# Kernel optimization log

Hardware: AMD Instinct MI355X
Metric: run time of the kernel (lower is better)

Reference implementation:

```python
import jax, jax.numpy as jnp
import numpy as np

DIM = 192
H = W = 128
HEADS = 6
HEAD_DIM = DIM // HEADS
WIN = 8
SHIFT = 4
B = 16
LN_EPS = 1e-5


def setup_inputs() -> dict:
    key = jax.random.key(0)
    ks = jax.random.split(key, 16)
    d = DIM
    s = lambda *sh: 1.0 / np.sqrt(sh[-1])
    inp = {
        "x": jax.random.normal(ks[0], (B, H * W, d), jnp.float32),
        # torch Linear layout: (out, in)
        "qkv_w": jax.random.normal(ks[1], (3 * d, d), jnp.float32) * s(d, d),
        "qkv_b": jnp.zeros((3 * d,), jnp.float32),
        "proj_w": jax.random.normal(ks[2], (d, d), jnp.float32) * s(d, d),
        "proj_b": jnp.zeros((d,), jnp.float32),
        "n1_g": jnp.ones((d,), jnp.float32),
        "n1_b": jnp.zeros((d,), jnp.float32),
        "n2_g": jnp.ones((d,), jnp.float32),
        "n2_b": jnp.zeros((d,), jnp.float32),
        "w1": jax.random.normal(ks[3], (4 * d, d), jnp.float32) * s(d, d),
        "b1": jnp.zeros((4 * d,), jnp.float32),
        "w2": jax.random.normal(ks[4], (d, 4 * d), jnp.float32) * s(d, 4 * d),
        "b2": jnp.zeros((d,), jnp.float32),
    }
    return inp


def _ln(x, g, b):
    m = jnp.mean(x, -1, keepdims=True)
    v = jnp.mean(jnp.square(x - m), -1, keepdims=True)
    return (x - m) * jax.lax.rsqrt(v + LN_EPS) * g + b


def _l2norm(x):
    n = jnp.sqrt(jnp.sum(jnp.square(x), -1, keepdims=True))
    return x / jnp.maximum(n, 1e-12)


def _swin_forward(x, qkv_w, qkv_b, proj_w, proj_b, n1_g, n1_b, n2_g, n2_b, w1, b1, w2, b2):
    Bq, L, C = x.shape
    shortcut = x
    h = _ln(x, n1_g, n1_b).reshape(Bq, H, W, C)
    h = jnp.roll(h, (-SHIFT, -SHIFT), axis=(1, 2))
    nH, nW = H // WIN, W // WIN
    hw = h.reshape(Bq, nH, WIN, nW, WIN, C).transpose(0, 1, 3, 2, 4, 5)
    hw = hw.reshape(Bq * nH * nW, WIN * WIN, C)
    N = WIN * WIN
    qkv = hw @ qkv_w.T + qkv_b                      # (nWin, N, 3C)
    qkv = qkv.reshape(-1, N, 3, HEADS, HEAD_DIM).transpose(2, 0, 3, 1, 4)
    q, k, v = qkv[0], qkv[1], qkv[2]                # (nWin, heads, N, hd)
    q = _l2norm(q)
    k = _l2norm(k)
    scale = HEAD_DIM ** -0.5
    attn = jnp.einsum('whnd,whmd->whnm', q, k) * scale
    attn = attn - jnp.max(attn, -1, keepdims=True)
    attn = jax.nn.softmax(attn, -1)
    attn = jnp.clip(attn, 1e-6, 1.0)
    o = jnp.einsum('whnm,whmd->whnd', attn, v)      # (nWin, heads, N, hd)
    o = o.transpose(0, 2, 1, 3).reshape(-1, N, C)
    o = o @ proj_w.T + proj_b
    # window reverse
    o = o.reshape(Bq, nH, nW, WIN, WIN, C).transpose(0, 1, 3, 2, 4, 5)
    o = o.reshape(Bq, H, W, C)
    o = jnp.roll(o, (SHIFT, SHIFT), axis=(1, 2)).reshape(Bq, L, C)
    x = shortcut + o
    m = _ln(x, n2_g, n2_b)
    m = jax.nn.gelu(m @ w1.T + b1, approximate=False) @ w2.T + b2
    return x + m


def reference(x, qkv_w, qkv_b, proj_w, proj_b, n1_g, n1_b, n2_g, n2_b, w1, b1, w2, b2):
    return _swin_forward(x, qkv_w, qkv_b, proj_w, proj_b, n1_g, n1_b, n2_g, n2_b, w1, b1, w2, b2)
```

## Files before the change

kernel.cpp:

```cpp
#include <hip/hip_runtime.h>


typedef short s8v __attribute__((ext_vector_type(8)));
typedef float f4v __attribute__((ext_vector_type(4)));
typedef unsigned short u16;

static __device__ __forceinline__ float b2f(u16 u) {
    unsigned int x = ((unsigned int)u) << 16;
    return __builtin_bit_cast(float, x);
}
static __device__ __forceinline__ u16 f2b(float f) {
    unsigned int u = __builtin_bit_cast(unsigned int, f);
    u = (u + 0x7FFF + ((u >> 16) & 1)) >> 16;
    return (u16)u;
}
static __device__ __forceinline__ f4v mfma16(s8v a, s8v b, f4v c) {
    return __builtin_amdgcn_mfma_f32_16x16x32_bf16(a, b, c, 0, 0, 0);
}

#define SWZ(r, e) ((e) ^ (((r) & 7) << 3))

#define SZ_QKV  110592
#define SZ_PROJ  36864
#define SZ_W1   147456
#define SZ_W2   147456
#define OFF_PROJ (SZ_QKV)
#define OFF_W1   (SZ_QKV + SZ_PROJ)
#define OFF_W2   (SZ_QKV + SZ_PROJ + SZ_W1)
#define W_TOTAL  (SZ_QKV + SZ_PROJ + SZ_W1 + SZ_W2)

__global__ __launch_bounds__(256) void cvt_weights(
    const float* __restrict__ qkv_w, const float* __restrict__ proj_w,
    const float* __restrict__ w1, const float* __restrict__ w2,
    u16* __restrict__ dst)
{
    int i4 = (blockIdx.x * 256 + threadIdx.x) * 4;
    const float* src; int off;
    if (i4 < OFF_PROJ)     { src = qkv_w; off = i4; }
    else if (i4 < OFF_W1)  { src = proj_w; off = i4 - OFF_PROJ; }
    else if (i4 < OFF_W2)  { src = w1; off = i4 - OFF_W1; }
    else                   { src = w2; off = i4 - OFF_W2; }
    float4 v = *(const float4*)(src + off);
    ushort4 o;
    o.x = f2b(v.x); o.y = f2b(v.y); o.z = f2b(v.z); o.w = f2b(v.w);
    *(ushort4*)(dst + i4) = o;
}

__global__ __launch_bounds__(256, 3) void attn_fused(
    const float* __restrict__ x, const u16* __restrict__ Wqkv,
    const float* __restrict__ bqkv, const u16* __restrict__ Wproj,
    const float* __restrict__ bproj, const float* __restrict__ g1,
    const float* __restrict__ bn1, const float* __restrict__ g2,
    const float* __restrict__ bn2, u16* __restrict__ x2,
    u16* __restrict__ xln)
{
    __shared__ __align__(16) u16 lds[27136];
    u16* hs   = lds;
    u16* ks   = lds;
    u16* vt   = lds + 12288;
    u16* pscr = lds + 24576;

    const int tid = threadIdx.x;
    const int wv = tid >> 6, lane = tid & 63;
    const int lr = lane & 15, lq = lane >> 4;
    const int wloc = blockIdx.x;
    const int bb = wloc >> 8, wh = (wloc >> 4) & 15, ww = wloc & 15;
    u16* pw = pscr + wv * 640;

    {
        int tk = tid >> 2, q4 = tid & 3;
        int gh = (wh * 8 + (tk >> 3) + 4) & 127;
        int gw = (ww * 8 + (tk & 7) + 4) & 127;
        const float* xr = x + (((size_t)bb * 128 + gh) * 128 + gw) * 192 + q4 * 48;
        float4 xv[12];
        float s = 0.f, sq = 0.f;
#pragma unroll
        for (int i = 0; i < 12; i++) {
            xv[i] = *(const float4*)(xr + i * 4);
            s += xv[i].x + xv[i].y + xv[i].z + xv[i].w;
            sq += xv[i].x * xv[i].x + xv[i].y * xv[i].y
                + xv[i].z * xv[i].z + xv[i].w * xv[i].w;
        }
        s += __shfl_xor(s, 1); sq += __shfl_xor(sq, 1);
        s += __shfl_xor(s, 2); sq += __shfl_xor(sq, 2);
        float mean = s * (1.0f / 192.0f);
        float var = sq * (1.0f / 192.0f) - mean * mean;
        float rstd = 1.0f / sqrtf(var + 1e-5f);
#pragma unroll
        for (int i = 0; i < 12; i += 2) {
            int c0 = q4 * 48 + i * 4;
            float4 ga  = *(const float4*)(g1 + c0);
            float4 gb  = *(const float4*)(g1 + c0 + 4);
            float4 ba  = *(const float4*)(bn1 + c0);
            float4 bbv = *(const float4*)(bn1 + c0 + 4);
            s8v ov;
            ov[0] = (short)f2b((xv[i].x - mean) * rstd * ga.x + ba.x);
            ov[1] = (short)f2b((xv[i].y - mean) * rstd * ga.y + ba.y);
            ov[2] = (short)f2b((xv[i].z - mean) * rstd * ga.z + ba.z);
            ov[3] = (short)f2b((xv[i].w - mean) * rstd * ga.w + ba.w);
            ov[4] = (short)f2b((xv[i + 1].x - mean) * rstd * gb.x + bbv.x);
            ov[5] = (short)f2b((xv[i + 1].y - mean) * rstd * gb.y + bbv.y);
            ov[6] = (short)f2b((xv[i + 1].z - mean) * rstd * gb.z + bbv.z);
            ov[7] = (short)f2b((xv[i + 1].w - mean) * rstd * gb.w + bbv.w);
            *(s8v*)&hs[SWZ(tk, tk * 192 + c0)] = ov;
        }
    }
    __syncthreads();

    const int trow = 16 * wv + lr;
    s8v af[6];
#pragma unroll
    for (int k = 0; k < 6; k++)
        af[k] = *(const s8v*)&hs[SWZ(trow, trow * 192 + 32 * k + lq * 8)];
    __syncthreads();

    s8v aq[6];
#pragma unroll
    for (int h = 0; h < 6; h++) {
        f4v acc[6] = {};
#pragma unroll
        for (int k = 0; k < 6; k++) {
#pragma unroll
            for (int n = 0; n < 6; n++) {
                int wr = (n < 2) ? (32 * h + 16 * n + lr)
                       : (n < 4) ? (192 + 32 * h + 16 * (n - 2) + lr)
                                 : (384 + 32 * h + 16 * (n - 4) + lr);
                s8v bf = *(const s8v*)&Wqkv[(size_t)wr * 192 + 32 * k + lq * 8];
                acc[n] = mfma16(af[k], bf, acc[n]);
            }
        }
        float bq0 = bqkv[32 * h + lr],       bq1 = bqkv[32 * h + 16 + lr];
        float bk0 = bqkv[192 + 32 * h + lr], bk1 = bqkv[192 + 32 * h + 16 + lr];
        float bv0 = bqkv[384 + 32 * h + lr], bv1 = bqkv[384 + 32 * h + 16 + lr];
#pragma unroll
        for (int reg = 0; reg < 4; reg++) {
            int row = 16 * wv + lq * 4 + reg;
            float q0 = acc[0][reg] + bq0, q1 = acc[1][reg] + bq1;
            float ss = q0 * q0 + q1 * q1;
#pragma unroll
            for (int m = 1; m < 16; m <<= 1) ss += __shfl_xor(ss, m);
            float inv = 1.0f / fmaxf(sqrtf(ss), 1e-12f);
            pw[(lq * 4 + reg) * 40 + lr]      = f2b(q0 * inv);
            pw[(lq * 4 + reg) * 40 + 16 + lr] = f2b(q1 * inv);

            float k0v = acc[2][reg] + bk0, k1v = acc[3][reg] + bk1;
            ss = k0v * k0v + k1v * k1v;
#pragma unroll
            for (int m = 1; m < 16; m <<= 1) ss += __shfl_xor(ss, m);
            inv = 1.0f / fmaxf(sqrtf(ss), 1e-12f);
            ks[SWZ(row, row * 192 + 32 * h + lr)]      = f2b(k0v * inv);
            ks[SWZ(row, row * 192 + 32 * h + 16 + lr)] = f2b(k1v * inv);

            int d0 = 32 * h + lr, d1 = 32 * h + 16 + lr;
            vt[SWZ(d0, d0 * 64 + row)] = f2b(acc[4][reg] + bv0);
            vt[SWZ(d1, d1 * 64 + row)] = f2b(acc[5][reg] + bv1);
        }
        aq[h] = *(const s8v*)&pw[lr * 40 + lq * 8];
    }
    __syncthreads();

    f4v acc2[12] = {};
    const float scale = 0.17677669529663687f;
#pragma unroll
    for (int h = 0; h < 6; h++) {
        f4v accS[4] = {};
#pragma unroll
        for (int j = 0; j < 4; j++) {
            int kr = 16 * j + lr;
            s8v bk = *(const s8v*)&ks[SWZ(kr, kr * 192 + 32 * h + lq * 8)];
            accS[j] = mfma16(aq[h], bk, accS[j]);
        }
        float p[4][4];
#pragma unroll
        for (int reg = 0; reg < 4; reg++) {
            float v0 = accS[0][reg] * scale, v1 = accS[1][reg] * scale;
            float v2 = accS[2][reg] * scale, v3 = accS[3][reg] * scale;
            float mx = fmaxf(fmaxf(v0, v1), fmaxf(v2, v3));
#pragma unroll
            for (int m = 1; m < 16; m <<= 1) mx = fmaxf(mx, __shfl_xor(mx, m));
            float e0 = __expf(v0 - mx), e1 = __expf(v1 - mx);
            float e2 = __expf(v2 - mx), e3 = __expf(v3 - mx);
            float sum = e0 + e1 + e2 + e3;
#pragma unroll
            for (int m = 1; m < 16; m <<= 1) sum += __shfl_xor(sum, m);
            float is = 1.0f / sum;
            p[0][reg] = fminf(fmaxf(e0 * is, 1e-6f), 1.0f);
            p[1][reg] = fminf(fmaxf(e1 * is, 1e-6f), 1.0f);
            p[2][reg] = fminf(fmaxf(e2 * is, 1e-6f), 1.0f);
            p[3][reg] = fminf(fmaxf(e3 * is, 1e-6f), 1.0f);
        }
        f4v accO[2] = {};
#pragma unroll
        for (int reg = 0; reg < 4; reg++) {
            pw[(lq * 4 + reg) * 40 + lr]      = f2b(p[0][reg]);
            pw[(lq * 4 + reg) * 40 + 16 + lr] = f2b(p[1][reg]);
        }
        {
            s8v ap0 = *(const s8v*)&pw[lr * 40 + lq * 8];
#pragma unroll
            for (int n = 0; n < 2; n++) {
                int d = 32 * h + 16 * n + lr;
                s8v bvf = *(const s8v*)&vt[SWZ(d, d * 64 + lq * 8)];
                accO[n] = mfma16(ap0, bvf, accO[n]);
            }
        }
#pragma unroll
        for (int reg = 0; reg < 4; reg++) {
            pw[(lq * 4 + reg) * 40 + lr]      = f2b(p[2][reg]);
            pw[(lq * 4 + reg) * 40 + 16 + lr] = f2b(p[3][reg]);
        }
        {
            s8v ap1 = *(const s8v*)&pw[lr * 40 + lq * 8];
#pragma unroll
            for (int n = 0; n < 2; n++) {
                int d = 32 * h + 16 * n + lr;
                s8v bvf = *(const s8v*)&vt[SWZ(d, d * 64 + 32 + lq * 8)];
                accO[n] = mfma16(ap1, bvf, accO[n]);
            }
        }
#pragma unroll
        for (int n = 0; n < 2; n++)
#pragma unroll
            for (int reg = 0; reg < 4; reg++)
                pw[(lq * 4 + reg) * 40 + 16 * n + lr] = f2b(accO[n][reg]);
        s8v apj = *(const s8v*)&pw[lr * 40 + lq * 8];
#pragma unroll
        for (int n = 0; n < 12; n++) {
            s8v bpj = *(const s8v*)&Wproj[(size_t)(16 * n + lr) * 192 + 32 * h + lq * 8];
            acc2[n] = mfma16(apj, bpj, acc2[n]);
        }
    }

    float bpv[12], g2v[12], b2v[12];
#pragma unroll
    for (int n = 0; n < 12; n++) {
        int col = 16 * n + lr;
        bpv[n] = bproj[col]; g2v[n] = g2[col]; b2v[n] = bn2[col];
    }
#pragma unroll
    for (int reg = 0; reg < 4; reg++) {
        int tk = 16 * wv + lq * 4 + reg;
        int gh = (wh * 8 + (tk >> 3) + 4) & 127;
        int gw = (ww * 8 + (tk & 7) + 4) & 127;
        size_t base = (((size_t)bb * 128 + gh) * 128 + gw) * 192;
        float vv[12];
        float s = 0.f, sq = 0.f;
#pragma unroll
        for (int n = 0; n < 12; n++) {
            float v = acc2[n][reg] + bpv[n] + x[base + 16 * n + lr];
            vv[n] = v; s += v; sq += v * v;
        }
        s += __shfl_xor(s, 1); sq += __shfl_xor(sq, 1);
        s += __shfl_xor(s, 2); sq += __shfl_xor(sq, 2);
        s += __shfl_xor(s, 4); sq += __shfl_xor(sq, 4);
        s += __shfl_xor(s, 8); sq += __shfl_xor(sq, 8);
        float mean = s * (1.0f / 192.0f);
        float var = sq * (1.0f / 192.0f) - mean * mean;
        float rstd = 1.0f / sqrtf(var + 1e-5f);
#pragma unroll
        for (int n = 0; n < 12; n++) {
            size_t idx = base + 16 * n + lr;
            x2[idx]  = f2b(vv[n]);
            xln[idx] = f2b((vv[n] - mean) * rstd * g2v[n] + b2v[n]);
        }
    }
}

__global__ __launch_bounds__(256, 3) void mlp1_gemm(
    const u16* __restrict__ xln, const u16* __restrict__ W1,
    const float* __restrict__ B1, u16* __restrict__ mh, int ldm, int nchunk)
{
    __shared__ __align__(16) u16 As[128 * 200];
    const int tid = threadIdx.x;
    const int wv = tid >> 6, lane = tid & 63;
    const int lr = lane & 15, lq = lane >> 4;
    const size_t m0 = (size_t)blockIdx.x * 128;

    {
        int r = tid >> 1, hf = tid & 1;
        const u16* xr = xln + (m0 + r) * 192 + hf * 96;
        u16* ar = As + r * 200 + hf * 96;
#pragma unroll
        for (int i = 0; i < 12; i++)
            *(s8v*)(ar + i * 8) = *(const s8v*)(xr + i * 8);
    }
    __syncthreads();

    for (int c = 0; c < nchunk; c++) {
        f4v acc[2][12] = {};
        for (int k0 = 0; k0 < 192; k0 += 32) {
            s8v afr[2];
#pragma unroll
            for (int mt = 0; mt < 2; mt++)
                afr[mt] = *(const s8v*)&As[(32 * wv + 16 * mt + lr) * 200 + k0 + lq * 8];
#pragma unroll
            for (int n = 0; n < 12; n++) {
                s8v bf = *(const s8v*)&W1[(size_t)(c * 192 + 16 * n + lr) * 192 + k0 + lq * 8];
#pragma unroll
                for (int mt = 0; mt < 2; mt++)
                    acc[mt][n] = mfma16(afr[mt], bf, acc[mt][n]);
            }
        }
#pragma unroll
        for (int n = 0; n < 12; n++) {
            int col = c * 192 + 16 * n + lr;
            float bb = B1[col];
#pragma unroll
            for (int mt = 0; mt < 2; mt++)
#pragma unroll
                for (int reg = 0; reg < 4; reg++) {
                    size_t row = m0 + 32 * wv + 16 * mt + lq * 4 + reg;
                    float v = acc[mt][n][reg] + bb;
                    v = 0.5f * v * (1.0f + erff(v * 0.70710678118654752f));
                    mh[row * ldm + col] = f2b(v);
                }
        }
    }
}

#define BM 128
#define BN 64
#define LDT 40

template <int RES>
__global__ __launch_bounds__(256) void gemm_bt(
    const u16* __restrict__ A, int lda,
    const u16* __restrict__ W, int ldb,
    const float* __restrict__ bias,
    const u16* __restrict__ residB, const float* __restrict__ residF, int ldr,
    float* __restrict__ Cout, int ldc, int K)
{
    __shared__ __align__(16) u16 As[BM * LDT];
    __shared__ __align__(16) u16 Bs[BN * LDT];
    const int tid = threadIdx.x;
    const int wave = tid >> 6, lane = tid & 63;
    const int lr = lane & 15, lq = lane >> 4;
    const int wm = (wave >> 1) * 64;
    const int wn = (wave & 1) * 32;
    const size_t m0 = (size_t)blockIdx.y * BM;
    const int n0 = blockIdx.x * BN;

    const int ar = tid >> 1, ac = (tid & 1) * 16;
    const int br = tid >> 2, bc = (tid & 3) * 8;
    const u16* aptr = A + (m0 + ar) * (size_t)lda + ac;
    const u16* bptr = W + (size_t)(n0 + br) * ldb + bc;

    f4v acc[4][2] = {};
    for (int k0 = 0; k0 < K; k0 += 32) {
        __syncthreads();
        *(s8v*)&As[ar * LDT + ac]     = *(const s8v*)(aptr + k0);
        *(s8v*)&As[ar * LDT + ac + 8] = *(const s8v*)(aptr + k0 + 8);
        *(s8v*)&Bs[br * LDT + bc]     = *(const s8v*)(bptr + k0);
        __syncthreads();
        s8v af[4], bfr[2];
#pragma unroll
        for (int mt = 0; mt < 4; mt++)
            af[mt] = *(const s8v*)&As[(wm + mt * 16 + lr) * LDT + lq * 8];
#pragma unroll
        for (int nt = 0; nt < 2; nt++)
            bfr[nt] = *(const s8v*)&Bs[(wn + nt * 16 + lr) * LDT + lq * 8];
#pragma unroll
        for (int mt = 0; mt < 4; mt++)
#pragma unroll
            for (int nt = 0; nt < 2; nt++)
                acc[mt][nt] = mfma16(af[mt], bfr[nt], acc[mt][nt]);
    }

    float bv[2];
#pragma unroll
    for (int nt = 0; nt < 2; nt++) {
        int col = n0 + wn + nt * 16 + lr;
        bv[nt] = bias ? bias[col] : 0.0f;
    }
#pragma unroll
    for (int mt = 0; mt < 4; mt++)
#pragma unroll
        for (int reg = 0; reg < 4; reg++) {
            size_t row = m0 + wm + mt * 16 + lq * 4 + reg;
#pragma unroll
            for (int nt = 0; nt < 2; nt++) {
                int col = n0 + wn + nt * 16 + lr;
                float v = acc[mt][nt][reg] + bv[nt];
                if (RES == 1) v += b2f(residB[row * (size_t)ldr + col]);
                if (RES == 2) v += residF[row * (size_t)ldr + col];
                Cout[row * (size_t)ldc + col] = v;
            }
        }
}

extern "C" void kernel_launch(void* const* d_in, const int* in_sizes, int n_in,
                              void* d_out, int out_size, void* d_ws, size_t ws_size,
                              hipStream_t stream) {
    const float* x      = (const float*)d_in[0];
    const float* qkv_w  = (const float*)d_in[1];
    const float* qkv_b  = (const float*)d_in[2];
    const float* proj_w = (const float*)d_in[3];
    const float* proj_b = (const float*)d_in[4];
    const float* n1_g   = (const float*)d_in[5];
    const float* n1_b   = (const float*)d_in[6];
    const float* n2_g   = (const float*)d_in[7];
    const float* n2_b   = (const float*)d_in[8];
    const float* w1     = (const float*)d_in[9];
    const float* b1     = (const float*)d_in[10];
    const float* w2     = (const float*)d_in[11];
    const float* b2     = (const float*)d_in[12];
    float* out = (float*)d_out;

    u16* wsu = (u16*)d_ws;
    u16* wQ  = wsu;
    u16* wP  = wsu + OFF_PROJ;
    u16* wW1 = wsu + OFF_W1;
    u16* wW2 = wsu + OFF_W2;
    char* dataBase = (char*)d_ws + (1 << 20);
    size_t avail = (ws_size > (1 << 20)) ? ws_size - (1 << 20) : 0;

    dim3 blk(256);
    cvt_weights<<<W_TOTAL / 1024, blk, 0, stream>>>(qkv_w, proj_w, w1, w2, wsu);

    const size_t perTok = (size_t)(192 + 192 + 768) * 2;
    int Bs = 16;
    while (Bs > 1 && (size_t)Bs * 16384 * perTok > avail) Bs >>= 1;
    const bool bigHC = ((size_t)Bs * 16384 * perTok <= avail);

    if (bigHC) {
        const int nslice = 16 / Bs;
        const size_t stok = (size_t)Bs * 16384;
        u16* x2buf  = (u16*)dataBase;
        u16* xlnbuf = x2buf + stok * 192;
        u16* mhbuf  = xlnbuf + stok * 192;
        for (int s = 0; s < nslice; s++) {
            const float* xs = x + (size_t)s * stok * 192;
            float* outs = out + (size_t)s * stok * 192;
            attn_fused<<<Bs * 256, blk, 0, stream>>>(xs, wQ, qkv_b, wP, proj_b,
                                                     n1_g, n1_b, n2_g, n2_b,
                                                     x2buf, xlnbuf);
            mlp1_gemm<<<Bs * 128, blk, 0, stream>>>(xlnbuf, wW1, b1, mhbuf, 768, 4);
            gemm_bt<1><<<dim3(3, Bs * 128), blk, 0, stream>>>(
                mhbuf, 768, wW2, 768, b2, x2buf, nullptr, 192, outs, 192, 768);
        }
    } else {
        const size_t stok = 16384;
        u16* x2buf  = (u16*)dataBase;
        u16* xlnbuf = x2buf + stok * 192;
        u16* mhbuf  = xlnbuf + stok * 192;
        for (int s = 0; s < 16; s++) {
            const float* xs = x + (size_t)s * stok * 192;
            float* outs = out + (size_t)s * stok * 192;
            attn_fused<<<256, blk, 0, stream>>>(xs, wQ, qkv_b, wP, proj_b,
                                                n1_g, n1_b, n2_g, n2_b,
                                                x2buf, xlnbuf);
            for (int c = 0; c < 4; c++) {
                mlp1_gemm<<<128, blk, 0, stream>>>(
                    xlnbuf, wW1 + (size_t)c * 192 * 192, b1 + c * 192,
                    mhbuf, 192, 1);
                if (c == 0)
                    gemm_bt<1><<<dim3(3, 128), blk, 0, stream>>>(
                        mhbuf, 192, wW2 + c * 192, 768, b2,
                        x2buf, nullptr, 192, outs, 192, 192);
                else
                    gemm_bt<2><<<dim3(3, 128), blk, 0, stream>>>(
                        mhbuf, 192, wW2 + c * 192, 768, nullptr,
                        nullptr, outs, 192, outs, 192, 192);
            }
        }
    }
}
```

Baseline: 1.659 ms.

## Fuse MLP into one kernel and pipeline per-head attention with smaller LDS

The MLP's two GEMMs become a single kernel. It keeps the GELU hidden chunk in shared memory and accumulates the second GEMM in registers, so the large hidden activation buffer is no longer written to and read back from global memory. The attention kernel now processes heads in a software pipeline. It computes QKV for head h while running attention for head h-1, using double-buffered per-head K/V slices. This shrinks LDS so occupancy can go from 3 to 4 blocks per CU, at the cost of one block-wide barrier per head and weight reloads per 64-row MLP tile.

```diff
diff --git a/kernel.cpp b/kernel.cpp
--- a/kernel.cpp
+++ b/kernel.cpp
@@ -46,7 +46,125 @@
     *(ushort4*)(dst + i4) = o;
 }
 
-__global__ __launch_bounds__(256, 3) void attn_fused(
+static __device__ __forceinline__ void qkv_head(
+    int h, const s8v* af, const u16* __restrict__ Wqkv,
+    const float* __restrict__ bqkv, u16* kb, u16* vb, u16* qw,
+    s8v& aqOut, int wv, int lr, int lq)
+{
+    f4v acc[6] = {};
+#pragma unroll
+    for (int k = 0; k < 6; k++) {
+#pragma unroll
+        for (int n = 0; n < 6; n++) {
+            int wr = (n < 2) ? (32 * h + 16 * n + lr)
+                   : (n < 4) ? (192 + 32 * h + 16 * (n - 2) + lr)
+                             : (384 + 32 * h + 16 * (n - 4) + lr);
+            s8v bf = *(const s8v*)&Wqkv[(size_t)wr * 192 + 32 * k + lq * 8];
+            acc[n] = mfma16(af[k], bf, acc[n]);
+        }
+    }
+    float bq0 = bqkv[32 * h + lr],       bq1 = bqkv[32 * h + 16 + lr];
+    float bk0 = bqkv[192 + 32 * h + lr], bk1 = bqkv[192 + 32 * h + 16 + lr];
+    float bv0 = bqkv[384 + 32 * h + lr], bv1 = bqkv[384 + 32 * h + 16 + lr];
+#pragma unroll
+    for (int reg = 0; reg < 4; reg++) {
+        int row = 16 * wv + lq * 4 + reg;
+        float q0 = acc[0][reg] + bq0, q1 = acc[1][reg] + bq1;
+        float ss = q0 * q0 + q1 * q1;
+#pragma unroll
+        for (int m = 1; m < 16; m <<= 1) ss += __shfl_xor(ss, m);
+        float inv = 1.0f / fmaxf(sqrtf(ss), 1e-12f);
+        qw[(lq * 4 + reg) * 40 + lr]      = f2b(q0 * inv);
+        qw[(lq * 4 + reg) * 40 + 16 + lr] = f2b(q1 * inv);
+
+        float k0v = acc[2][reg] + bk0, k1v = acc[3][reg] + bk1;
+        ss = k0v * k0v + k1v * k1v;
+#pragma unroll
+        for (int m = 1; m < 16; m <<= 1) ss += __shfl_xor(ss, m);
+        inv = 1.0f / fmaxf(sqrtf(ss), 1e-12f);
+        kb[SWZ(row, row * 32 + lr)]      = f2b(k0v * inv);
+        kb[SWZ(row, row * 32 + 16 + lr)] = f2b(k1v * inv);
+
+        vb[SWZ(lr, lr * 64 + row)]             = f2b(acc[4][reg] + bv0);
+        vb[SWZ(16 + lr, (16 + lr) * 64 + row)] = f2b(acc[5][reg] + bv1);
+    }
+    aqOut = *(const s8v*)&qw[lr * 40 + lq * 8];
+}
+
+static __device__ __forceinline__ void attn_head(
+    int h, s8v aq, const u16* kb, const u16* vb, u16* pw,
+    f4v* acc2, const u16* __restrict__ Wproj, int wv, int lr, int lq)
+{
+    f4v accS[4] = {};
+#pragma unroll
+    for (int j = 0; j < 4; j++) {
+        int kr = 16 * j + lr;
+        s8v bk = *(const s8v*)&kb[SWZ(kr, kr * 32 + lq * 8)];
+        accS[j] = mfma16(aq, bk, accS[j]);
+    }
+    const float scale = 0.17677669529663687f;
+    float p[4][4];
+#pragma unroll
+    for (int reg = 0; reg < 4; reg++) {
+        float v0 = accS[0][reg] * scale, v1 = accS[1][reg] * scale;
+        float v2 = accS[2][reg] * scale, v3 = accS[3][reg] * scale;
+        float mx = fmaxf(fmaxf(v0, v1), fmaxf(v2, v3));
+#pragma unroll
+        for (int m = 1; m < 16; m <<= 1) mx = fmaxf(mx, __shfl_xor(mx, m));
+        float e0 = __expf(v0 - mx), e1 = __expf(v1 - mx);
+        float e2 = __expf(v2 - mx), e3 = __expf(v3 - mx);
+        float sum = e0 + e1 + e2 + e3;
+#pragma unroll
+        for (int m = 1; m < 16; m <<= 1) sum += __shfl_xor(sum, m);
+        float is = 1.0f / sum;
+        p[0][reg] = fminf(fmaxf(e0 * is, 1e-6f), 1.0f);
+        p[1][reg] = fminf(fmaxf(e1 * is, 1e-6f), 1.0f);
+        p[2][reg] = fminf(fmaxf(e2 * is, 1e-6f), 1.0f);
+        p[3][reg] = fminf(fmaxf(e3 * is, 1e-6f), 1.0f);
+    }
+    f4v accO[2] = {};
+#pragma unroll
+    for (int reg = 0; reg < 4; reg++) {
+        pw[(lq * 4 + reg) * 40 + lr]      = f2b(p[0][reg]);
+        pw[(lq * 4 + reg) * 40 + 16 + lr] = f2b(p[1][reg]);
+    }
+    {
+        s8v ap = *(const s8v*)&pw[lr * 40 + lq * 8];
+#pragma unroll
+        for (int n = 0; n < 2; n++) {
+            int d = 16 * n + lr;
+            s8v bvf = *(const s8v*)&vb[SWZ(d, d * 64 + lq * 8)];
+            accO[n] = mfma16(ap, bvf, accO[n]);
+        }
+    }
+#pragma unroll
+    for (int reg = 0; reg < 4; reg++) {
+        pw[(lq * 4 + reg) * 40 + lr]      = f2b(p[2][reg]);
+        pw[(lq * 4 + reg) * 40 + 16 + lr] = f2b(p[3][reg]);
+    }
+    {
+        s8v ap = *(const s8v*)&pw[lr * 40 + lq * 8];
+#pragma unroll
+        for (int n = 0; n < 2; n++) {
+            int d = 16 * n + lr;
+            s8v bvf = *(const s8v*)&vb[SWZ(d, d * 64 + 32 + lq * 8)];
+            accO[n] = mfma16(ap, bvf, accO[n]);
+        }
+    }
+#pragma unroll
+    for (int n = 0; n < 2; n++)
+#pragma unroll
+        for (int reg = 0; reg < 4; reg++)
+            pw[(lq * 4 + reg) * 40 + 16 * n + lr] = f2b(accO[n][reg]);
+    s8v apj = *(const s8v*)&pw[lr * 40 + lq * 8];
+#pragma unroll
+    for (int n = 0; n < 12; n++) {
+        s8v bpj = *(const s8v*)&Wproj[(size_t)(16 * n + lr) * 192 + 32 * h + lq * 8];
+        acc2[n] = mfma16(apj, bpj, acc2[n]);
+    }
+}
+
+__global__ __launch_bounds__(256, 4) void attn_fused(
     const float* __restrict__ x, const u16* __restrict__ Wqkv,
     const float* __restrict__ bqkv, const u16* __restrict__ Wproj,
     const float* __restrict__ bproj, const float* __restrict__ g1,
@@ -54,17 +172,17 @@
     const float* __restrict__ bn2, u16* __restrict__ x2,
     u16* __restrict__ xln)
 {
-    __shared__ __align__(16) u16 lds[27136];
+    __shared__ __align__(16) u16 lds[13312];
     u16* hs   = lds;
-    u16* ks   = lds;
-    u16* vt   = lds + 12288;
-    u16* pscr = lds + 24576;
+    u16* qscr = lds + 8192;
+    u16* pscr = lds + 10752;
 
     const int tid = threadIdx.x;
     const int wv = tid >> 6, lane = tid & 63;
     const int lr = lane & 15, lq = lane >> 4;
     const int wloc = blockIdx.x;
     const int bb = wloc >> 8, wh = (wloc >> 4) & 15, ww = wloc & 15;
+    u16* qw = qscr + wv * 640;
     u16* pw = pscr + wv * 640;
 
     {
@@ -105,8 +223,6 @@
             *(s8v*)&hs[SWZ(tk, tk * 192 + c0)] = ov;
         }
     }
-    __syncthreads();
-
     const int trow = 16 * wv + lr;
     s8v af[6];
 #pragma unroll
@@ -114,122 +230,21 @@
         af[k] = *(const s8v*)&hs[SWZ(trow, trow * 192 + 32 * k + lq * 8)];
     __syncthreads();
 
-    s8v aq[6];
+    f4v acc2[12] = {};
+    s8v aqv[6];
 #pragma unroll
     for (int h = 0; h < 6; h++) {
-        f4v acc[6] = {};
-#pragma unroll
-        for (int k = 0; k < 6; k++) {
-#pragma unroll
-            for (int n = 0; n < 6; n++) {
-                int wr = (n < 2) ? (32 * h + 16 * n + lr)
-                       : (n < 4) ? (192 + 32 * h + 16 * (n - 2) + lr)
-                                 : (384 + 32 * h + 16 * (n - 4) + lr);
-                s8v bf = *(const s8v*)&Wqkv[(size_t)wr * 192 + 32 * k + lq * 8];
-                acc[n] = mfma16(af[k], bf, acc[n]);
-            }
-        }
-        float bq0 = bqkv[32 * h + lr],       bq1 = bqkv[32 * h + 16 + lr];
-        float bk0 = bqkv[192 + 32 * h + lr], bk1 = bqkv[192 + 32 * h + 16 + lr];
-        float bv0 = bqkv[384 + 32 * h + lr], bv1 = bqkv[384 + 32 * h + 16 + lr];
-#pragma unroll
-        for (int reg = 0; reg < 4; reg++) {
-            int row = 16 * wv + lq * 4 + reg;
-            float q0 = acc[0][reg] + bq0, q1 = acc[1][reg] + bq1;
-            float ss = q0 * q0 + q1 * q1;
-#pragma unroll
-            for (int m = 1; m < 16; m <<= 1) ss += __shfl_xor(ss, m);
-            float inv = 1.0f / fmaxf(sqrtf(ss), 1e-12f);
-            pw[(lq * 4 + reg) * 40 + lr]      = f2b(q0 * inv);
-            pw[(lq * 4 + reg) * 40 + 16 + lr] = f2b(q1 * inv);
-
-            float k0v = acc[2][reg] + bk0, k1v = acc[3][reg] + bk1;
-            ss = k0v * k0v + k1v * k1v;
-#pragma unroll
-            for (int m = 1; m < 16; m <<= 1) ss += __shfl_xor(ss, m);
-            inv = 1.0f / fmaxf(sqrtf(ss), 1e-12f);
-            ks[SWZ(row, row * 192 + 32 * h + lr)]      = f2b(k0v * inv);
-            ks[SWZ(row, row * 192 + 32 * h + 16 + lr)] = f2b(k1v * inv);
-
-            int d0 = 32 * h + lr, d1 = 32 * h + 16 + lr;
-            vt[SWZ(d0, d0 * 64 + row)] = f2b(acc[4][reg] + bv0);
-            vt[SWZ(d1, d1 * 64 + row)] = f2b(acc[5][reg] + bv1);
-        }
-        aq[h] = *(const s8v*)&pw[lr * 40 + lq * 8];
-    }
-    __syncthreads();
-
-    f4v acc2[12] = {};
-    const float scale = 0.17677669529663687f;
-#pragma unroll
-    for (int h = 0; h < 6; h++) {
-        f4v accS[4] = {};
-#pragma unroll
-        for (int j = 0; j < 4; j++) {
-            int kr = 16 * j + lr;
-            s8v bk = *(const s8v*)&ks[SWZ(kr, kr * 192 + 32 * h + lq * 8)];
-            accS[j] = mfma16(aq[h], bk, accS[j]);
-        }
-        float p[4][4];
-#pragma unroll
-        for (int reg = 0; reg < 4; reg++) {
-            float v0 = accS[0][reg] * scale, v1 = accS[1][reg] * scale;
-            float v2 = accS[2][reg] * scale, v3 = accS[3][reg] * scale;
-            float mx = fmaxf(fmaxf(v0, v1), fmaxf(v2, v3));
-#pragma unroll
-            for (int m = 1; m < 16; m <<= 1) mx = fmaxf(mx, __shfl_xor(mx, m));
-            float e0 = __expf(v0 - mx), e1 = __expf(v1 - mx);
-            float e2 = __expf(v2 - mx), e3 = __expf(v3 - mx);
-            float sum = e0 + e1 + e2 + e3;
-#pragma unroll
-            for (int m = 1; m < 16; m <<= 1) sum += __shfl_xor(sum, m);
-            float is = 1.0f / sum;
-            p[0][reg] = fminf(fmaxf(e0 * is, 1e-6f), 1.0f);
-            p[1][reg] = fminf(fmaxf(e1 * is, 1e-6f), 1.0f);
-            p[2][reg] = fminf(fmaxf(e2 * is, 1e-6f), 1.0f);
-            p[3][reg] = fminf(fmaxf(e3 * is, 1e-6f), 1.0f);
-        }
-        f4v accO[2] = {};
-#pragma unroll
-        for (int reg = 0; reg < 4; reg++) {
-            pw[(lq * 4 + reg) * 40 + lr]      = f2b(p[0][reg]);
-            pw[(lq * 4 + reg) * 40 + 16 + lr] = f2b(p[1][reg]);
-        }
-        {
-            s8v ap0 = *(const s8v*)&pw[lr * 40 + lq * 8];
-#pragma unroll
-            for (int n = 0; n < 2; n++) {
-                int d = 32 * h + 16 * n + lr;
-                s8v bvf = *(const s8v*)&vt[SWZ(d, d * 64 + lq * 8)];
-                accO[n] = mfma16(ap0, bvf, accO[n]);
-            }
-        }
-#pragma unroll
-        for (int reg = 0; reg < 4; reg++) {
-            pw[(lq * 4 + reg) * 40 + lr]      = f2b(p[2][reg]);
-            pw[(lq * 4 + reg) * 40 + 16 + lr] = f2b(p[3][reg]);
-        }
-        {
-            s8v ap1 = *(const s8v*)&pw[lr * 40 + lq * 8];
-#pragma unroll
-            for (int n = 0; n < 2; n++) {
-                int d = 32 * h + 16 * n + lr;
-                s8v bvf = *(const s8v*)&vt[SWZ(d, d * 64 + 32 + lq * 8)];
-                accO[n] = mfma16(ap1, bvf, accO[n]);
-            }
-        }
-#pragma unroll
-        for (int n = 0; n < 2; n++)
-#pragma unroll
-            for (int reg = 0; reg < 4; reg++)
-                pw[(lq * 4 + reg) * 40 + 16 * n + lr] = f2b(accO[n][reg]);
-        s8v apj = *(const s8v*)&pw[lr * 40 + lq * 8];
-#pragma unroll
-        for (int n = 0; n < 12; n++) {
-            s8v bpj = *(const s8v*)&Wproj[(size_t)(16 * n + lr) * 192 + 32 * h + lq * 8];
-            acc2[n] = mfma16(apj, bpj, acc2[n]);
-        }
-    }
+        u16* kb = lds + ((h & 1) << 11);
+        u16* vb = lds + 4096 + ((h & 1) << 11);
+        qkv_head(h, af, Wqkv, bqkv, kb, vb, qw, aqv[h], wv, lr, lq);
+        if (h > 0) {
+            u16* kbp = lds + (((h - 1) & 1) << 11);
+            u16* vbp = lds + 4096 + (((h - 1) & 1) << 11);
+            attn_head(h - 1, aqv[h - 1], kbp, vbp, pw, acc2, Wproj, wv, lr, lq);
+        }
+        __syncthreads();
+    }
+    attn_head(5, aqv[5], lds + 2048, lds + 4096 + 2048, pw, acc2, Wproj, wv, lr, lq);
 
     float bpv[12], g2v[12], b2v[12];
 #pragma unroll
@@ -266,126 +281,77 @@
     }
 }
 
-__global__ __launch_bounds__(256, 3) void mlp1_gemm(
-    const u16* __restrict__ xln, const u16* __restrict__ W1,
-    const float* __restrict__ B1, u16* __restrict__ mh, int ldm, int nchunk)
+__global__ __launch_bounds__(256, 3) void mlp_fused(
+    const u16* __restrict__ xln, const u16* __restrict__ x2,
+    const u16* __restrict__ W1, const float* __restrict__ B1,
+    const u16* __restrict__ W2, const float* __restrict__ B2,
+    float* __restrict__ out)
 {
-    __shared__ __align__(16) u16 As[128 * 200];
+    __shared__ __align__(16) u16 lds[24576];
+    u16* As = lds;
+    u16* Ms = lds + 12288;
     const int tid = threadIdx.x;
     const int wv = tid >> 6, lane = tid & 63;
     const int lr = lane & 15, lq = lane >> 4;
-    const size_t m0 = (size_t)blockIdx.x * 128;
+    const size_t m0 = (size_t)blockIdx.x * 64;
 
     {
-        int r = tid >> 1, hf = tid & 1;
-        const u16* xr = xln + (m0 + r) * 192 + hf * 96;
-        u16* ar = As + r * 200 + hf * 96;
-#pragma unroll
-        for (int i = 0; i < 12; i++)
-            *(s8v*)(ar + i * 8) = *(const s8v*)(xr + i * 8);
+        int r = tid >> 2, q4 = tid & 3;
+        const u16* xr = xln + (m0 + r) * 192 + q4 * 48;
+        int ebase = r * 192 + q4 * 48;
+#pragma unroll
+        for (int i = 0; i < 6; i++)
+            *(s8v*)&As[SWZ(r, ebase + i * 8)] = *(const s8v*)(xr + i * 8);
     }
     __syncthreads();
 
-    for (int c = 0; c < nchunk; c++) {
-        f4v acc[2][12] = {};
-        for (int k0 = 0; k0 < 192; k0 += 32) {
-            s8v afr[2];
-#pragma unroll
-            for (int mt = 0; mt < 2; mt++)
-                afr[mt] = *(const s8v*)&As[(32 * wv + 16 * mt + lr) * 200 + k0 + lq * 8];
+    f4v facc[12] = {};
+    const int arow = 16 * wv + lr;
+#pragma unroll
+    for (int c = 0; c < 4; c++) {
+        f4v g[12] = {};
+#pragma unroll
+        for (int k = 0; k < 6; k++) {
+            s8v a = *(const s8v*)&As[SWZ(arow, arow * 192 + 32 * k + lq * 8)];
 #pragma unroll
             for (int n = 0; n < 12; n++) {
-                s8v bf = *(const s8v*)&W1[(size_t)(c * 192 + 16 * n + lr) * 192 + k0 + lq * 8];
-#pragma unroll
-                for (int mt = 0; mt < 2; mt++)
-                    acc[mt][n] = mfma16(afr[mt], bf, acc[mt][n]);
+                s8v bf = *(const s8v*)&W1[(size_t)(c * 192 + 16 * n + lr) * 192 + 32 * k + lq * 8];
+                g[n] = mfma16(a, bf, g[n]);
             }
         }
 #pragma unroll
         for (int n = 0; n < 12; n++) {
-            int col = c * 192 + 16 * n + lr;
-            float bb = B1[col];
-#pragma unroll
-            for (int mt = 0; mt < 2; mt++)
-#pragma unroll
-                for (int reg = 0; reg < 4; reg++) {
-                    size_t row = m0 + 32 * wv + 16 * mt + lq * 4 + reg;
-                    float v = acc[mt][n][reg] + bb;
-                    v = 0.5f * v * (1.0f + erff(v * 0.70710678118654752f));
-                    mh[row * ldm + col] = f2b(v);
-                }
-        }
-    }
-}
-
-#define BM 128
-#define BN 64
-#define LDT 40
-
-template <int RES>
-__global__ __launch_bounds__(256) void gemm_bt(
-    const u16* __restrict__ A, int lda,
-    const u16* __restrict__ W, int ldb,
-    const float* __restrict__ bias,
-    const u16* __restrict__ residB, const float* __restrict__ residF, int ldr,
-    float* __restrict__ Cout, int ldc, int K)
-{
-    __shared__ __align__(16) u16 As[BM * LDT];
-    __shared__ __align__(16) u16 Bs[BN * LDT];
-    const int tid = threadIdx.x;
-    const int wave = tid >> 6, lane = tid & 63;
-    const int lr = lane & 15, lq = lane >> 4;
-    const int wm = (wave >> 1) * 64;
-    const int wn = (wave & 1) * 32;
-    const size_t m0 = (size_t)blockIdx.y * BM;
-    const int n0 = blockIdx.x * BN;
-
-    const int ar = tid >> 1, ac = (tid & 1) * 16;
-    const int br = tid >> 2, bc = (tid & 3) * 8;
-    const u16* aptr = A + (m0 + ar) * (size_t)lda + ac;
-    const u16* bptr = W + (size_t)(n0 + br) * ldb + bc;
-
-    f4v acc[4][2] = {};
-    for (int k0 = 0; k0 < K; k0 += 32) {
-        __syncthreads();
-        *(s8v*)&As[ar * LDT + ac]     = *(const s8v*)(aptr + k0);
-        *(s8v*)&As[ar * LDT + ac + 8] = *(const s8v*)(aptr + k0 + 8);
-        *(s8v*)&Bs[br * LDT + bc]     = *(const s8v*)(bptr + k0);
-        __syncthreads();
-        s8v af[4], bfr[2];
-#pragma unroll
-        for (int mt = 0; mt < 4; mt++)
-            af[mt] = *(const s8v*)&As[(wm + mt * 16 + lr) * LDT + lq * 8];
-#pragma unroll
-        for (int nt = 0; nt < 2; nt++)
-            bfr[nt] = *(const s8v*)&Bs[(wn + nt * 16 + lr) * LDT + lq * 8];
-#pragma unroll
-        for (int mt = 0; mt < 4; mt++)
-#pragma unroll
-            for (int nt = 0; nt < 2; nt++)
-                acc[mt][nt] = mfma16(af[mt], bfr[nt], acc[mt][nt]);
-    }
-
-    float bv[2];
-#pragma unroll
-    for (int nt = 0; nt < 2; nt++) {
-        int col = n0 + wn + nt * 16 + lr;
-        bv[nt] = bias ? bias[col] : 0.0f;
-    }
-#pragma unroll
-    for (int mt = 0; mt < 4; mt++)
+            int col = 16 * n + lr;
+            float bb = B1[c * 192 + col];
+#pragma unroll
+            for (int reg = 0; reg < 4; reg++) {
+                int row = 16 * wv + lq * 4 + reg;
+                float v = g[n][reg] + bb;
+                v = 0.5f * v * (1.0f + erff(v * 0.70710678118654752f));
+                Ms[SWZ(row, row * 192 + col)] = f2b(v);
+            }
+        }
+#pragma unroll
+        for (int k = 0; k < 6; k++) {
+            s8v a2 = *(const s8v*)&Ms[SWZ(arow, arow * 192 + 32 * k + lq * 8)];
+#pragma unroll
+            for (int n = 0; n < 12; n++) {
+                s8v bf = *(const s8v*)&W2[(size_t)(16 * n + lr) * 768 + c * 192 + 32 * k + lq * 8];
+                facc[n] = mfma16(a2, bf, facc[n]);
+            }
+        }
+    }
+
+#pragma unroll
+    for (int n = 0; n < 12; n++) {
+        int col = 16 * n + lr;
+        float bb = B2[col];
 #pragma unroll
         for (int reg = 0; reg < 4; reg++) {
-            size_t row = m0 + wm + mt * 16 + lq * 4 + reg;
-#pragma unroll
-            for (int nt = 0; nt < 2; nt++) {
-                int col = n0 + wn + nt * 16 + lr;
-                float v = acc[mt][nt][reg] + bv[nt];
-                if (RES == 1) v += b2f(residB[row * (size_t)ldr + col]);
-                if (RES == 2) v += residF[row * (size_t)ldr + col];
-                Cout[row * (size_t)ldc + col] = v;
-            }
-        }
+            size_t row = m0 + 16 * wv + lq * 4 + reg;
+            out[row * 192 + col] = facc[n][reg] + bb + b2f(x2[row * 192 + col]);
+        }
+    }
 }
 
 extern "C" void kernel_launch(void* const* d_in, const int* in_sizes, int n_in,
@@ -417,51 +383,21 @@
     dim3 blk(256);
     cvt_weights<<<W_TOTAL / 1024, blk, 0, stream>>>(qkv_w, proj_w, w1, w2, wsu);
 
-    const size_t perTok = (size_t)(192 + 192 + 768) * 2;
+    const size_t perTok = (size_t)(192 + 192) * 2;
     int Bs = 16;
     while (Bs > 1 && (size_t)Bs * 16384 * perTok > avail) Bs >>= 1;
-    const bool bigHC = ((size_t)Bs * 16384 * perTok <= avail);
-
-    if (bigHC) {
-        const int nslice = 16 / Bs;
-        const size_t stok = (size_t)Bs * 16384;
-        u16* x2buf  = (u16*)dataBase;
-        u16* xlnbuf = x2buf + stok * 192;
-        u16* mhbuf  = xlnbuf + stok * 192;
-        for (int s = 0; s < nslice; s++) {
-            const float* xs = x + (size_t)s * stok * 192;
-            float* outs = out + (size_t)s * stok * 192;
-            attn_fused<<<Bs * 256, blk, 0, stream>>>(xs, wQ, qkv_b, wP, proj_b,
-                                                     n1_g, n1_b, n2_g, n2_b,
-                                                     x2buf, xlnbuf);
-            mlp1_gemm<<<Bs * 128, blk, 0, stream>>>(xlnbuf, wW1, b1, mhbuf, 768, 4);
-            gemm_bt<1><<<dim3(3, Bs * 128), blk, 0, stream>>>(
-                mhbuf, 768, wW2, 768, b2, x2buf, nullptr, 192, outs, 192, 768);
-        }
-    } else {
-        const size_t stok = 16384;
-        u16* x2buf  = (u16*)dataBase;
-        u16* xlnbuf = x2buf + stok * 192;
-        u16* mhbuf  = xlnbuf + stok * 192;
-        for (int s = 0; s < 16; s++) {
-            const float* xs = x + (size_t)s * stok * 192;
-            float* outs = out + (size_t)s * stok * 192;
-            attn_fused<<<256, blk, 0, stream>>>(xs, wQ, qkv_b, wP, proj_b,
-                                                n1_g, n1_b, n2_g, n2_b,
-                                                x2buf, xlnbuf);
-            for (int c = 0; c < 4; c++) {
-                mlp1_gemm<<<128, blk, 0, stream>>>(
-                    xlnbuf, wW1 + (size_t)c * 192 * 192, b1 + c * 192,
-                    mhbuf, 192, 1);
-                if (c == 0)
-                    gemm_bt<1><<<dim3(3, 128), blk, 0, stream>>>(
-                        mhbuf, 192, wW2 + c * 192, 768, b2,
-                        x2buf, nullptr, 192, outs, 192, 192);
-                else
-                    gemm_bt<2><<<dim3(3, 128), blk, 0, stream>>>(
-                        mhbuf, 192, wW2 + c * 192, 768, nullptr,
-                        nullptr, outs, 192, outs, 192, 192);
-            }
-        }
-    }
-}
+    const int nslice = 16 / Bs;
+    const size_t stok = (size_t)Bs * 16384;
+    u16* x2buf  = (u16*)dataBase;
+    u16* xlnbuf = x2buf + stok * 192;
+
+    for (int s = 0; s < nslice; s++) {
+        const float* xs = x + (size_t)s * stok * 192;
+        float* outs = out + (size_t)s * stok * 192;
+        attn_fused<<<Bs * 256, blk, 0, stream>>>(xs, wQ, qkv_b, wP, proj_b,
+                                                 n1_g, n1_b, n2_g, n2_b,
+                                                 x2buf, xlnbuf);
+        mlp_fused<<<Bs * 256, blk, 0, stream>>>(xlnbuf, x2buf, wW1, b1,
+                                                wW2, b2, outs);
+    }
+}
```

New measurement: 2.543 ms. 53.3% more time.
